# Optimization experiments

Measured on AMD Instinct MI355X. Metric: run time of the kernel, lower is better.

## Reference

```python
import jax, jax.numpy as jnp
import numpy as np

B, H, W, IMG_CH = 64, 16, 16, 1024
N, TEXT_CH = 256, 768
FQ = FK = 512


def _glorot(key, shape, fan_in, fan_out):
    lim = np.sqrt(6.0 / (fan_in + fan_out)).astype(np.float32)
    return jax.random.uniform(key, shape, jnp.float32, -lim, lim)


def setup_inputs() -> dict:
    key = jax.random.key(0)
    ks = jax.random.split(key, 8)
    x1 = jax.random.normal(ks[0], (B, H, W, IMG_CH), jnp.float32)
    x2 = jax.random.normal(ks[1], (B, N, TEXT_CH), jnp.float32)
    # padding mask over text tokens, broadcast over image pixels
    masks = (jax.random.uniform(ks[2], (B, N, 1)) > 0.1).astype(jnp.float32)
    kernel_q = _glorot(ks[3], (1, 1, IMG_CH, FQ), IMG_CH, FQ)
    kernel_k = _glorot(ks[4], (1, TEXT_CH, FK), TEXT_CH, FK)
    kernel_v = _glorot(ks[5], (1, TEXT_CH, IMG_CH), TEXT_CH, IMG_CH)
    kernel_o = _glorot(ks[6], (1, 1, IMG_CH, IMG_CH), IMG_CH, IMG_CH)
    return {
        "x1": x1, "x2": x2, "masks": masks,
        "kernel_q": kernel_q, "bias_q": jnp.zeros((FQ,), jnp.float32),
        "kernel_k": kernel_k, "bias_k": jnp.zeros((FK,), jnp.float32),
        "kernel_v": kernel_v, "bias_v": jnp.zeros((IMG_CH,), jnp.float32),
        "kernel_o": kernel_o, "bias_o": jnp.zeros((IMG_CH,), jnp.float32),
    }


def reference(x1, x2, masks, kernel_q, bias_q, kernel_k, bias_k,
              kernel_v, bias_v, kernel_o, bias_o):
    b, h, w, c = x1.shape
    # 1x1 conv2d == pointwise matmul over channels
    q = jnp.einsum('bhwc,cf->bhwf', x1, kernel_q[0, 0]) + bias_q   # (B,H,W,512)
    # width-1 conv1d == pointwise matmul over channels
    k = jnp.einsum('bnc,cf->bnf', x2, kernel_k[0]) + bias_k        # (B,N,512)
    v = jnp.einsum('bnc,cf->bnf', x2, kernel_v[0]) + bias_v        # (B,N,IMG_CH)
    qf = q.reshape(b, h * w, -1)                                   # (B,HW,512)
    s = jnp.einsum('bqd,bnd->bqn', qf, k)                          # (B,HW,N)
    beta = jax.nn.softmax(s, axis=-1)
    # NON-STANDARD: mask applied AFTER softmax (no renormalization)
    beta = beta * jnp.swapaxes(masks, 1, 2)                        # (B,HW,N)*(B,1,N)
    o = jnp.einsum('bqn,bnf->bqf', beta, v).reshape(b, h, w, c)    # (B,H,W,IMG_CH)
    o = jnp.einsum('bhwc,cf->bhwf', o, kernel_o[0, 0]) + bias_o
    return o, beta
```

## Files before the change

kernel.cpp:

```cpp
#include <hip/hip_runtime.h>
#include <hip/hip_bf16.h>

using bf16 = __hip_bfloat16;

typedef __attribute__((ext_vector_type(8))) short short8;
typedef __attribute__((ext_vector_type(4))) float f32x4;

#define MFMA_BF16(a, b, c) __builtin_amdgcn_mfma_f32_16x16x32_bf16((a), (b), (c), 0, 0, 0)

__device__ __forceinline__ void lds_load16(const void* g, void* l) {
    __builtin_amdgcn_global_load_lds(
        (const __attribute__((address_space(1))) void*)g,
        (__attribute__((address_space(3))) void*)l, 16, 0, 0);
}

template <int N>
__device__ __forceinline__ void waitvm() {
    asm volatile("s_waitcnt vmcnt(%0)" ::"n"(N) : "memory");
}
__device__ __forceinline__ void lgkm0_fence() {
    asm volatile("s_waitcnt lgkmcnt(0)" ::: "memory");
}

__device__ __forceinline__ void swiz_xcd(int& bx, int& by) {
    const int NX = gridDim.x, NY = gridDim.y;
    const int flat = blockIdx.y * NX + blockIdx.x;
    const int cid = flat & 7, slot = flat >> 3;
    by = cid * (NY >> 3) + slot / NX;
    bx = slot % NX;
}

__device__ __forceinline__ void stage_bf16_128(const bf16* src, int ld, bf16* tile,
                                               int wave, int lane) {
    const int r = lane >> 2;
    const int c = ((lane & 3) ^ ((r >> 1) & 3)) * 8;
#pragma unroll
    for (int p = 0; p < 2; ++p) {
        const int row = p * 64 + wave * 16;
        lds_load16(src + (size_t)(row + r) * ld + c, tile + row * 32);
    }
}
__device__ __forceinline__ void stage_bf16_256_w8(const bf16* src, int ld, bf16* tile,
                                                  int wave, int lane) {
    const int r = lane >> 2;
    const int c = ((lane & 3) ^ ((r >> 1) & 3)) * 8;
#pragma unroll
    for (int p = 0; p < 2; ++p) {
        const int row = p * 128 + wave * 16;
        lds_load16(src + (size_t)(row + r) * ld + c, tile + row * 32);
    }
}
__device__ __forceinline__ void stage_f32_128(const float* src, int ld, float* tile,
                                              int wave, int lane) {
    const int r = lane >> 3;
    const int c = ((lane & 7) ^ r) * 4;
#pragma unroll
    for (int it = 0; it < 4; ++it) {
        const int row = it * 32 + wave * 8;
        lds_load16(src + (size_t)(row + r) * ld + c, tile + row * 32);
    }
}

__device__ __forceinline__ short8 rd_bf16(const bf16* tile, int row, int quad) {
    const int c = (quad ^ ((row >> 1) & 3)) * 8;
    return *(const short8*)(tile + row * 32 + c);
}
template <bool SPLIT>
__device__ __forceinline__ void rd_f32_hilo(const float* tile, int row, int quad,
                                            short8& h, short8& l) {
    const int f = row & 7;
    const f32x4 x0 = *(const f32x4*)(tile + row * 32 + ((2 * quad) ^ f) * 4);
    const f32x4 x1 = *(const f32x4*)(tile + row * 32 + ((2 * quad + 1) ^ f) * 4);
    float xs[8] = {x0[0], x0[1], x0[2], x0[3], x1[0], x1[1], x1[2], x1[3]};
#pragma unroll
    for (int j = 0; j < 8; ++j) {
        const bf16 hb = __float2bfloat16(xs[j]);
        h[j] = *(const short*)&hb;
        if constexpr (SPLIT) {
            const bf16 lb = __float2bfloat16(xs[j] - __bfloat162float(hb));
            l[j] = *(const short*)&lb;
        }
    }
}

template <bool SPLIT>
__global__ void transpose_split(const float* __restrict__ in, bf16* __restrict__ outh,
                                bf16* __restrict__ outl, int K, int N) {
    __shared__ float t[32][33];
    const int n0 = blockIdx.x * 32, k0 = blockIdx.y * 32;
    const int tx = threadIdx.x, ty = threadIdx.y;
#pragma unroll
    for (int i = 0; i < 4; ++i)
        t[ty + i * 8][tx] = in[(size_t)(k0 + ty + i * 8) * N + n0 + tx];
    __syncthreads();
#pragma unroll
    for (int i = 0; i < 4; ++i) {
        const float x = t[tx][ty + i * 8];
        const bf16 hb = __float2bfloat16(x);
        const size_t idx = (size_t)(n0 + ty + i * 8) * K + k0 + tx;
        outh[idx] = hb;
        if constexpr (SPLIT) outl[idx] = __float2bfloat16(x - __bfloat162float(hb));
    }
}

enum { G_SPLIT3 = 0, G_VT = 1, G_F32 = 2, G_PV = 3 };

template <int MODE>
__global__ __launch_bounds__(256) void gemm2(
    const void* __restrict__ Av, const bf16* __restrict__ Bth,
    const bf16* __restrict__ Btl, const float* __restrict__ bias,
    void* __restrict__ out0, void* __restrict__ out1, int N, int K) {
    constexpr bool ASPLIT = (MODE == G_SPLIT3);
    constexpr bool ACONV = (MODE == G_SPLIT3 || MODE == G_VT);
    constexpr int SZ_A = ACONV ? 128 * 32 * 4 : 128 * 32 * 2;
    constexpr int SZ_B = 128 * 32 * 2;
    constexpr int STAGE = SZ_A + SZ_B + (ASPLIT ? SZ_B : 0);
    constexpr int DBUF = 2 * STAGE;
    constexpr int SMEM =
        (MODE == G_VT) ? (DBUF > 128 * 136 * 2 ? DBUF : 128 * 136 * 2) : DBUF;
    constexpr int SLOADS = ACONV ? (ASPLIT ? 8 : 6) : 4;
    __shared__ __align__(16) char smem[SMEM];
    bf16* Ts = (bf16*)smem;

    const int tid = threadIdx.x, wave = tid >> 6, lane = tid & 63;
    const int quad = lane >> 4, l15 = lane & 15;
    const int wr = wave >> 1, wc = wave & 1;

    int bx, by;
    if constexpr (MODE == G_PV) {
        bx = blockIdx.x;
        by = blockIdx.y;
    } else {
        swiz_xcd(bx, by);
    }
    const int m0 = by * 128, n0 = bx * 128;
    const int z = blockIdx.z;

    const float* Af = (const float*)Av;
    const bf16* Ab = (const bf16*)Av;
    const bf16* Bh = Bth;
    if constexpr (MODE == G_PV) {
        Ab += (size_t)z * 256 * 256;
        Bh += (size_t)z * 1024 * 256;
    }

    auto do_stage = [&](int k0, char* base) {
        if constexpr (ACONV)
            stage_f32_128(Af + (size_t)m0 * K + k0, K, (float*)base, wave, lane);
        else
            stage_bf16_128(Ab + (size_t)m0 * K + k0, K, (bf16*)base, wave, lane);
        stage_bf16_128(Bh + (size_t)n0 * K + k0, K, (bf16*)(base + SZ_A), wave, lane);
        if constexpr (ASPLIT)
            stage_bf16_128(Btl + (size_t)n0 * K + k0, K, (bf16*)(base + SZ_A + SZ_B),
                           wave, lane);
    };

    f32x4 acc[4][4] = {};
    const int nt = K / 32;
    do_stage(0, smem);
    do_stage(32, smem + STAGE);
    int cur = 0;
    for (int t = 0; t < nt; ++t) {
        if (t + 1 < nt)
            waitvm<SLOADS>();
        else
            waitvm<0>();
        __builtin_amdgcn_s_barrier();

        char* base = smem + cur * STAGE;
        const float* AsF = (const float*)base;
        const bf16* AsH = (const bf16*)base;
        const bf16* BsH = (const bf16*)(base + SZ_A);
        const bf16* BsL = (const bf16*)(base + SZ_A + SZ_B);

        short8 ah[4], al[4], bh[4], bl[4];
#pragma unroll
        for (int tt = 0; tt < 4; ++tt) {
            const int ra = wr * 64 + tt * 16 + l15;
            const int rb = wc * 64 + tt * 16 + l15;
            if constexpr (ACONV)
                rd_f32_hilo<ASPLIT>(AsF, ra, quad, ah[tt], al[tt]);
            else
                ah[tt] = rd_bf16(AsH, ra, quad);
            bh[tt] = rd_bf16(BsH, rb, quad);
            if constexpr (ASPLIT) bl[tt] = rd_bf16(BsL, rb, quad);
        }
        lgkm0_fence();
        __builtin_amdgcn_s_barrier();
        if (t + 2 < nt) do_stage((t + 2) * 32, base);

        if constexpr (ASPLIT) {
#pragma unroll
            for (int ti = 0; ti < 4; ++ti)
#pragma unroll
                for (int tj = 0; tj < 4; ++tj) {
                    acc[ti][tj] = MFMA_BF16(al[ti], bh[tj], acc[ti][tj]);
                    acc[ti][tj] = MFMA_BF16(ah[ti], bl[tj], acc[ti][tj]);
                    acc[ti][tj] = MFMA_BF16(ah[ti], bh[tj], acc[ti][tj]);
                }
        } else {
#pragma unroll
            for (int ti = 0; ti < 4; ++ti)
#pragma unroll
                for (int tj = 0; tj < 4; ++tj)
                    acc[ti][tj] = MFMA_BF16(ah[ti], bh[tj], acc[ti][tj]);
        }
        cur ^= 1;
    }

    float bv4[4] = {0.f, 0.f, 0.f, 0.f};
    if constexpr (MODE != G_PV) {
#pragma unroll
        for (int tj = 0; tj < 4; ++tj) bv4[tj] = bias[n0 + wc * 64 + tj * 16 + l15];
    }

    if constexpr (MODE == G_VT) {
#pragma unroll
        for (int ti = 0; ti < 4; ++ti)
#pragma unroll
            for (int tj = 0; tj < 4; ++tj)
#pragma unroll
                for (int i = 0; i < 4; ++i) {
                    const int ml = wr * 64 + ti * 16 + quad * 4 + i;
                    const int nl = wc * 64 + tj * 16 + l15;
                    Ts[nl * 136 + ml] = __float2bfloat16(acc[ti][tj][i] + bv4[tj]);
                }
        __syncthreads();
        const int bIdx = m0 >> 8, tok0 = m0 & 255;
        const int nl = tid >> 1, half = tid & 1;
        bf16* dst = (bf16*)out0 + ((size_t)bIdx * N + n0 + nl) * 256 + tok0 + half * 64;
        const bf16* src = &Ts[nl * 136 + half * 64];
#pragma unroll
        for (int j = 0; j < 8; ++j)
            *(short8*)(dst + j * 8) = *(const short8*)(src + j * 8);
    } else {
#pragma unroll
        for (int ti = 0; ti < 4; ++ti)
#pragma unroll
            for (int tj = 0; tj < 4; ++tj)
#pragma unroll
                for (int i = 0; i < 4; ++i) {
                    const size_t row = m0 + wr * 64 + ti * 16 + quad * 4 + i;
                    const size_t col = n0 + wc * 64 + tj * 16 + l15;
                    const float v = acc[ti][tj][i] + bv4[tj];
                    if constexpr (MODE == G_F32) {
                        ((float*)out0)[row * N + col] = v;
                    } else if constexpr (MODE == G_PV) {
                        ((bf16*)out0)[((size_t)z * 256 + row) * N + col] =
                            __float2bfloat16(v);
                    } else {
                        const bf16 hb = __float2bfloat16(v);
                        ((bf16*)out0)[row * N + col] = hb;
                        ((bf16*)out1)[row * N + col] =
                            __float2bfloat16(v - __bfloat162float(hb));
                    }
                }
    }
}

__global__ __launch_bounds__(512) void attn_s(
    const bf16* __restrict__ qh, const bf16* __restrict__ ql,
    const bf16* __restrict__ kh, const bf16* __restrict__ kl,
    const float* __restrict__ masks, float* __restrict__ beta_out,
    bf16* __restrict__ betaB) {
    __shared__ bf16 kH[2][256 * 32], kL[2][256 * 32];
    __shared__ float redM[4][32], redS[4][32];
    int qt, b;
    swiz_xcd(qt, b);
    const int tid = threadIdx.x, wave = tid >> 6, lane = tid & 63;
    const int quad = lane >> 4, l15 = lane & 15;
    const int wr = wave >> 2, wq = wave & 3;

    f32x4 acc[4] = {};
    const size_t qoff = ((size_t)(b * 256 + qt * 32 + wr * 16 + l15)) * 512;
    const size_t kbase = (size_t)(b * 256) * 512;

    stage_bf16_256_w8(kh + kbase, 512, kH[0], wave, lane);
    stage_bf16_256_w8(kl + kbase, 512, kL[0], wave, lane);
    stage_bf16_256_w8(kh + kbase + 32, 512, kH[1], wave, lane);
    stage_bf16_256_w8(kl + kbase + 32, 512, kL[1], wave, lane);
    int cur = 0;
    for (int t = 0; t < 16; ++t) {
        const int k0 = t * 32;
        if (t + 1 < 16)
            waitvm<4>();
        else
            waitvm<0>();
        __builtin_amdgcn_s_barrier();

        const short8 aH = *(const short8*)(qh + qoff + k0 + quad * 8);
        const short8 aL = *(const short8*)(ql + qoff + k0 + quad * 8);
        short8 bH[4], bL[4];
#pragma unroll
        for (int nt = 0; nt < 4; ++nt) {
            const int kr = wq * 64 + nt * 16 + l15;
            bH[nt] = rd_bf16(kH[cur], kr, quad);
            bL[nt] = rd_bf16(kL[cur], kr, quad);
        }
        lgkm0_fence();
        __builtin_amdgcn_s_barrier();
        if (t + 2 < 16) {
            stage_bf16_256_w8(kh + kbase + (t + 2) * 32, 512, kH[cur], wave, lane);
            stage_bf16_256_w8(kl + kbase + (t + 2) * 32, 512, kL[cur], wave, lane);
        }
#pragma unroll
        for (int nt = 0; nt < 4; ++nt) {
            acc[nt] = MFMA_BF16(aH, bH[nt], acc[nt]);
            acc[nt] = MFMA_BF16(aH, bL[nt], acc[nt]);
            acc[nt] = MFMA_BF16(aL, bH[nt], acc[nt]);
        }
        cur ^= 1;
    }

    float pm[4], ps[4];
#pragma unroll
    for (int i = 0; i < 4; ++i) {
        float m = fmaxf(fmaxf(acc[0][i], acc[1][i]), fmaxf(acc[2][i], acc[3][i]));
#pragma unroll
        for (int s = 1; s < 16; s <<= 1) m = fmaxf(m, __shfl_xor(m, s));
        float sum = 0.f;
#pragma unroll
        for (int nt = 0; nt < 4; ++nt) sum += __expf(acc[nt][i] - m);
#pragma unroll
        for (int s = 1; s < 16; s <<= 1) sum += __shfl_xor(sum, s);
        pm[i] = m;
        ps[i] = sum;
    }
    if (l15 == 0) {
#pragma unroll
        for (int i = 0; i < 4; ++i) {
            redM[wq][wr * 16 + quad * 4 + i] = pm[i];
            redS[wq][wr * 16 + quad * 4 + i] = ps[i];
        }
    }
    __syncthreads();
    float gm[4], ginv[4];
#pragma unroll
    for (int i = 0; i < 4; ++i) {
        const int r = wr * 16 + quad * 4 + i;
        const float m = fmaxf(fmaxf(redM[0][r], redM[1][r]), fmaxf(redM[2][r], redM[3][r]));
        const float s = redS[0][r] * __expf(redM[0][r] - m) +
                        redS[1][r] * __expf(redM[1][r] - m) +
                        redS[2][r] * __expf(redM[2][r] - m) +
                        redS[3][r] * __expf(redM[3][r] - m);
        gm[i] = m;
        ginv[i] = 1.0f / s;
    }
#pragma unroll
    for (int nt = 0; nt < 4; ++nt) {
        const int col = wq * 64 + nt * 16 + l15;
        const float mv = masks[b * 256 + col];
#pragma unroll
        for (int i = 0; i < 4; ++i) {
            const int row = qt * 32 + wr * 16 + quad * 4 + i;
            const float bvv = __expf(acc[nt][i] - gm[i]) * ginv[i] * mv;
            const size_t idx = ((size_t)(b * 256 + row)) * 256 + col;
            beta_out[idx] = bvv;
            betaB[idx] = __float2bfloat16(bvv);
        }
    }
}

extern "C" void kernel_launch(void* const* d_in, const int* in_sizes, int n_in,
                              void* d_out, int out_size, void* d_ws, size_t ws_size,
                              hipStream_t stream) {
    const float* x1 = (const float*)d_in[0];
    const float* x2 = (const float*)d_in[1];
    const float* masks = (const float*)d_in[2];
    const float* Wq = (const float*)d_in[3];
    const float* bq = (const float*)d_in[4];
    const float* Wk = (const float*)d_in[5];
    const float* bk = (const float*)d_in[6];
    const float* Wv = (const float*)d_in[7];
    const float* bv = (const float*)d_in[8];
    const float* Wo = (const float*)d_in[9];
    const float* bo = (const float*)d_in[10];

    char* ws = (char*)d_ws;
    bf16* WqTh = (bf16*)(ws + 0);
    bf16* WqTl = (bf16*)(ws + 1048576);
    bf16* WkTh = (bf16*)(ws + 2097152);
    bf16* WkTl = (bf16*)(ws + 2883584);
    bf16* WvTh = (bf16*)(ws + 3670016);
    bf16* WoTh = (bf16*)(ws + 5242880);
    bf16* qh = (bf16*)(ws + 7340032);
    bf16* ql = (bf16*)(ws + 24117248);
    bf16* kh = (bf16*)(ws + 40894464);
    bf16* kl = (bf16*)(ws + 57671680);
    bf16* vT = (bf16*)(ws + 74448896);
    bf16* betaB = (bf16*)(ws + 108003328);
    bf16* o_mid = (bf16*)(ws + 7340032);

    float* out_o = (float*)d_out;
    float* out_beta = out_o + (size_t)16384 * 1024;

    const dim3 tb(32, 8);
    transpose_split<true><<<dim3(16, 32), tb, 0, stream>>>(Wq, WqTh, WqTl, 1024, 512);
    transpose_split<true><<<dim3(16, 24), tb, 0, stream>>>(Wk, WkTh, WkTl, 768, 512);
    transpose_split<false><<<dim3(32, 24), tb, 0, stream>>>(Wv, WvTh, nullptr, 768, 1024);
    transpose_split<false><<<dim3(32, 32), tb, 0, stream>>>(Wo, WoTh, nullptr, 1024, 1024);

    gemm2<G_SPLIT3><<<dim3(4, 128), 256, 0, stream>>>(x1, WqTh, WqTl, bq, qh, ql, 512, 1024);
    gemm2<G_SPLIT3><<<dim3(4, 128), 256, 0, stream>>>(x2, WkTh, WkTl, bk, kh, kl, 512, 768);
    gemm2<G_VT><<<dim3(8, 128), 256, 0, stream>>>(x2, WvTh, nullptr, bv, vT, nullptr, 1024, 768);

    attn_s<<<dim3(8, 64), 512, 0, stream>>>(qh, ql, kh, kl, masks, out_beta, betaB);

    gemm2<G_PV><<<dim3(8, 2, 64), 256, 0, stream>>>(betaB, vT, nullptr, nullptr, o_mid,
                                                    nullptr, 1024, 256);
    gemm2<G_F32><<<dim3(8, 128), 256, 0, stream>>>(o_mid, WoTh, nullptr, bo, out_o,
                                                   nullptr, 1024, 1024);
}
```

Measured before the change: 413.6 us.

## Use 8 waves per GEMM block with half-height per-wave tiles

The shared GEMM kernel goes from 4 waves (2x2, 64x64 per wave) to 8 waves (4x2, 32x64 per wave) per 128x128 block. Staging helpers are templated on row count and wave count, so each wave issues fewer async LDS loads and the vmcnt wait thresholds are halved to match. The aim is more waves per CU and fewer accumulator registers per wave, to hide memory and LDS latency. In exchange, B fragments are reread from LDS by twice as many waves, raising LDS traffic per MFMA.

```diff
diff --git a/kernel.cpp b/kernel.cpp
--- a/kernel.cpp
+++ b/kernel.cpp
@@ -30,33 +30,25 @@
     bx = slot % NX;
 }
 
-__device__ __forceinline__ void stage_bf16_128(const bf16* src, int ld, bf16* tile,
-                                               int wave, int lane) {
+template <int ROWS, int NW>
+__device__ __forceinline__ void stage_bf16(const bf16* src, int ld, bf16* tile,
+                                           int wave, int lane) {
     const int r = lane >> 2;
     const int c = ((lane & 3) ^ ((r >> 1) & 3)) * 8;
 #pragma unroll
-    for (int p = 0; p < 2; ++p) {
-        const int row = p * 64 + wave * 16;
+    for (int p = 0; p < ROWS / (16 * NW); ++p) {
+        const int row = p * (16 * NW) + wave * 16;
         lds_load16(src + (size_t)(row + r) * ld + c, tile + row * 32);
     }
 }
-__device__ __forceinline__ void stage_bf16_256_w8(const bf16* src, int ld, bf16* tile,
-                                                  int wave, int lane) {
-    const int r = lane >> 2;
-    const int c = ((lane & 3) ^ ((r >> 1) & 3)) * 8;
-#pragma unroll
-    for (int p = 0; p < 2; ++p) {
-        const int row = p * 128 + wave * 16;
-        lds_load16(src + (size_t)(row + r) * ld + c, tile + row * 32);
-    }
-}
-__device__ __forceinline__ void stage_f32_128(const float* src, int ld, float* tile,
-                                              int wave, int lane) {
+template <int ROWS, int NW>
+__device__ __forceinline__ void stage_f32(const float* src, int ld, float* tile,
+                                          int wave, int lane) {
     const int r = lane >> 3;
     const int c = ((lane & 7) ^ r) * 4;
 #pragma unroll
-    for (int it = 0; it < 4; ++it) {
-        const int row = it * 32 + wave * 8;
+    for (int p = 0; p < ROWS / (8 * NW); ++p) {
+        const int row = p * (8 * NW) + wave * 8;
         lds_load16(src + (size_t)(row + r) * ld + c, tile + row * 32);
     }
 }
@@ -106,7 +98,7 @@
 enum { G_SPLIT3 = 0, G_VT = 1, G_F32 = 2, G_PV = 3 };
 
 template <int MODE>
-__global__ __launch_bounds__(256) void gemm2(
+__global__ __launch_bounds__(512, 4) void gemm2(
     const void* __restrict__ Av, const bf16* __restrict__ Bth,
     const bf16* __restrict__ Btl, const float* __restrict__ bias,
     void* __restrict__ out0, void* __restrict__ out1, int N, int K) {
@@ -118,7 +110,7 @@
     constexpr int DBUF = 2 * STAGE;
     constexpr int SMEM =
         (MODE == G_VT) ? (DBUF > 128 * 136 * 2 ? DBUF : 128 * 136 * 2) : DBUF;
-    constexpr int SLOADS = ACONV ? (ASPLIT ? 8 : 6) : 4;
+    constexpr int SLOADS = ACONV ? (ASPLIT ? 4 : 3) : 2;
     __shared__ __align__(16) char smem[SMEM];
     bf16* Ts = (bf16*)smem;
 
@@ -146,16 +138,16 @@
 
     auto do_stage = [&](int k0, char* base) {
         if constexpr (ACONV)
-            stage_f32_128(Af + (size_t)m0 * K + k0, K, (float*)base, wave, lane);
+            stage_f32<128, 8>(Af + (size_t)m0 * K + k0, K, (float*)base, wave, lane);
         else
-            stage_bf16_128(Ab + (size_t)m0 * K + k0, K, (bf16*)base, wave, lane);
-        stage_bf16_128(Bh + (size_t)n0 * K + k0, K, (bf16*)(base + SZ_A), wave, lane);
+            stage_bf16<128, 8>(Ab + (size_t)m0 * K + k0, K, (bf16*)base, wave, lane);
+        stage_bf16<128, 8>(Bh + (size_t)n0 * K + k0, K, (bf16*)(base + SZ_A), wave, lane);
         if constexpr (ASPLIT)
-            stage_bf16_128(Btl + (size_t)n0 * K + k0, K, (bf16*)(base + SZ_A + SZ_B),
-                           wave, lane);
+            stage_bf16<128, 8>(Btl + (size_t)n0 * K + k0, K, (bf16*)(base + SZ_A + SZ_B),
+                               wave, lane);
     };
 
-    f32x4 acc[4][4] = {};
+    f32x4 acc[2][4] = {};
     const int nt = K / 32;
     do_stage(0, smem);
     do_stage(32, smem + STAGE);
@@ -173,15 +165,18 @@
         const bf16* BsH = (const bf16*)(base + SZ_A);
         const bf16* BsL = (const bf16*)(base + SZ_A + SZ_B);
 
-        short8 ah[4], al[4], bh[4], bl[4];
-#pragma unroll
-        for (int tt = 0; tt < 4; ++tt) {
-            const int ra = wr * 64 + tt * 16 + l15;
-            const int rb = wc * 64 + tt * 16 + l15;
+        short8 ah[2], al[2], bh[4], bl[4];
+#pragma unroll
+        for (int tt = 0; tt < 2; ++tt) {
+            const int ra = wr * 32 + tt * 16 + l15;
             if constexpr (ACONV)
                 rd_f32_hilo<ASPLIT>(AsF, ra, quad, ah[tt], al[tt]);
             else
                 ah[tt] = rd_bf16(AsH, ra, quad);
+        }
+#pragma unroll
+        for (int tt = 0; tt < 4; ++tt) {
+            const int rb = wc * 64 + tt * 16 + l15;
             bh[tt] = rd_bf16(BsH, rb, quad);
             if constexpr (ASPLIT) bl[tt] = rd_bf16(BsL, rb, quad);
         }
@@ -191,7 +186,7 @@
 
         if constexpr (ASPLIT) {
 #pragma unroll
-            for (int ti = 0; ti < 4; ++ti)
+            for (int ti = 0; ti < 2; ++ti)
 #pragma unroll
                 for (int tj = 0; tj < 4; ++tj) {
                     acc[ti][tj] = MFMA_BF16(al[ti], bh[tj], acc[ti][tj]);
@@ -200,7 +195,7 @@
                 }
         } else {
 #pragma unroll
-            for (int ti = 0; ti < 4; ++ti)
+            for (int ti = 0; ti < 2; ++ti)
 #pragma unroll
                 for (int tj = 0; tj < 4; ++tj)
                     acc[ti][tj] = MFMA_BF16(ah[ti], bh[tj], acc[ti][tj]);
@@ -216,31 +211,32 @@
 
     if constexpr (MODE == G_VT) {
 #pragma unroll
-        for (int ti = 0; ti < 4; ++ti)
+        for (int ti = 0; ti < 2; ++ti)
 #pragma unroll
             for (int tj = 0; tj < 4; ++tj)
 #pragma unroll
                 for (int i = 0; i < 4; ++i) {
-                    const int ml = wr * 64 + ti * 16 + quad * 4 + i;
+                    const int ml = wr * 32 + ti * 16 + quad * 4 + i;
                     const int nl = wc * 64 + tj * 16 + l15;
                     Ts[nl * 136 + ml] = __float2bfloat16(acc[ti][tj][i] + bv4[tj]);
                 }
         __syncthreads();
         const int bIdx = m0 >> 8, tok0 = m0 & 255;
-        const int nl = tid >> 1, half = tid & 1;
-        bf16* dst = (bf16*)out0 + ((size_t)bIdx * N + n0 + nl) * 256 + tok0 + half * 64;
-        const bf16* src = &Ts[nl * 136 + half * 64];
-#pragma unroll
-        for (int j = 0; j < 8; ++j)
+        const int nl = tid >> 2, qtr = tid & 3;
+        bf16* dst =
+            (bf16*)out0 + ((size_t)bIdx * N + n0 + nl) * 256 + tok0 + qtr * 32;
+        const bf16* src = &Ts[nl * 136 + qtr * 32];
+#pragma unroll
+        for (int j = 0; j < 4; ++j)
             *(short8*)(dst + j * 8) = *(const short8*)(src + j * 8);
     } else {
 #pragma unroll
-        for (int ti = 0; ti < 4; ++ti)
+        for (int ti = 0; ti < 2; ++ti)
 #pragma unroll
             for (int tj = 0; tj < 4; ++tj)
 #pragma unroll
                 for (int i = 0; i < 4; ++i) {
-                    const size_t row = m0 + wr * 64 + ti * 16 + quad * 4 + i;
+                    const size_t row = m0 + wr * 32 + ti * 16 + quad * 4 + i;
                     const size_t col = n0 + wc * 64 + tj * 16 + l15;
                     const float v = acc[ti][tj][i] + bv4[tj];
                     if constexpr (MODE == G_F32) {
@@ -275,10 +271,10 @@
     const size_t qoff = ((size_t)(b * 256 + qt * 32 + wr * 16 + l15)) * 512;
     const size_t kbase = (size_t)(b * 256) * 512;
 
-    stage_bf16_256_w8(kh + kbase, 512, kH[0], wave, lane);
-    stage_bf16_256_w8(kl + kbase, 512, kL[0], wave, lane);
-    stage_bf16_256_w8(kh + kbase + 32, 512, kH[1], wave, lane);
-    stage_bf16_256_w8(kl + kbase + 32, 512, kL[1], wave, lane);
+    stage_bf16<256, 8>(kh + kbase, 512, kH[0], wave, lane);
+    stage_bf16<256, 8>(kl + kbase, 512, kL[0], wave, lane);
+    stage_bf16<256, 8>(kh + kbase + 32, 512, kH[1], wave, lane);
+    stage_bf16<256, 8>(kl + kbase + 32, 512, kL[1], wave, lane);
     int cur = 0;
     for (int t = 0; t < 16; ++t) {
         const int k0 = t * 32;
@@ -300,8 +296,8 @@
         lgkm0_fence();
         __builtin_amdgcn_s_barrier();
         if (t + 2 < 16) {
-            stage_bf16_256_w8(kh + kbase + (t + 2) * 32, 512, kH[cur], wave, lane);
-            stage_bf16_256_w8(kl + kbase + (t + 2) * 32, 512, kL[cur], wave, lane);
+            stage_bf16<256, 8>(kh + kbase + (t + 2) * 32, 512, kH[cur], wave, lane);
+            stage_bf16<256, 8>(kl + kbase + (t + 2) * 32, 512, kL[cur], wave, lane);
         }
 #pragma unroll
         for (int nt = 0; nt < 4; ++nt) {
@@ -400,14 +396,14 @@
     transpose_split<false><<<dim3(32, 24), tb, 0, stream>>>(Wv, WvTh, nullptr, 768, 1024);
     transpose_split<false><<<dim3(32, 32), tb, 0, stream>>>(Wo, WoTh, nullptr, 1024, 1024);
 
-    gemm2<G_SPLIT3><<<dim3(4, 128), 256, 0, stream>>>(x1, WqTh, WqTl, bq, qh, ql, 512, 1024);
-    gemm2<G_SPLIT3><<<dim3(4, 128), 256, 0, stream>>>(x2, WkTh, WkTl, bk, kh, kl, 512, 768);
-    gemm2<G_VT><<<dim3(8, 128), 256, 0, stream>>>(x2, WvTh, nullptr, bv, vT, nullptr, 1024, 768);
+    gemm2<G_SPLIT3><<<dim3(4, 128), 512, 0, stream>>>(x1, WqTh, WqTl, bq, qh, ql, 512, 1024);
+    gemm2<G_SPLIT3><<<dim3(4, 128), 512, 0, stream>>>(x2, WkTh, WkTl, bk, kh, kl, 512, 768);
+    gemm2<G_VT><<<dim3(8, 128), 512, 0, stream>>>(x2, WvTh, nullptr, bv, vT, nullptr, 1024, 768);
 
     attn_s<<<dim3(8, 64), 512, 0, stream>>>(qh, ql, kh, kl, masks, out_beta, betaB);
 
-    gemm2<G_PV><<<dim3(8, 2, 64), 256, 0, stream>>>(betaB, vT, nullptr, nullptr, o_mid,
+    gemm2<G_PV><<<dim3(8, 2, 64), 512, 0, stream>>>(betaB, vT, nullptr, nullptr, o_mid,
                                                     nullptr, 1024, 256);
-    gemm2<G_F32><<<dim3(8, 128), 256, 0, stream>>>(o_mid, WoTh, nullptr, bo, out_o,
+    gemm2<G_F32><<<dim3(8, 128), 512, 0, stream>>>(o_mid, WoTh, nullptr, bo, out_o,
                                                    nullptr, 1024, 1024);
 }
```

After: 414.6 us. About the same (+0.2%).
